# Performance work log

Measured on AMD Instinct MI355X. Metric: run time of the kernel, lower is better.

Reference implementation:

```python
import jax, jax.numpy as jnp
import numpy as np

V, E, H, T = 100000, 128, 256, 7
B, S = 64, 512
START, STOP = 5, 6
H2 = H // 2


def setup_inputs() -> dict:
    key = jax.random.key(0)
    ks = jax.random.split(key, 16)
    rn = lambda k, shape, s=0.1: jax.random.normal(k, shape, jnp.float32) * s
    inp = {}
    inp["sentence"] = jax.random.randint(ks[0], (B, S), 0, V)
    inp["tags"] = jax.random.randint(ks[1], (B, S), 0, 5)
    inp["h0"] = jax.random.normal(ks[2], (2, B, H2), jnp.float32)
    inp["c0"] = jax.random.normal(ks[3], (2, B, H2), jnp.float32)
    inp["embedding"] = rn(ks[4], (V, E), 1.0)
    inp["w_ih_f"] = rn(ks[5], (4 * H2, E)); inp["w_hh_f"] = rn(ks[6], (4 * H2, H2))
    inp["b_ih_f"] = rn(ks[7], (4 * H2,)); inp["b_hh_f"] = rn(ks[8], (4 * H2,))
    inp["w_ih_b"] = rn(ks[9], (4 * H2, E)); inp["w_hh_b"] = rn(ks[10], (4 * H2, H2))
    inp["b_ih_b"] = rn(ks[11], (4 * H2,)); inp["b_hh_b"] = rn(ks[12], (4 * H2,))
    inp["w_out"] = rn(ks[13], (T, H)); inp["b_out"] = rn(ks[14], (T,))
    trans = jax.random.normal(ks[15], (T, T), jnp.float32)
    trans = trans.at[START, :].set(-10000.0).at[:, STOP].set(-10000.0)
    inp["transitions"] = trans
    return inp


def _lstm_dir(x, h0, c0, wih, whh, bih, bhh, reverse):
    # x: [S, B, E]; PyTorch gate order i, f, g, o
    def step(carry, xt):
        h, c = carry
        z = xt @ wih.T + h @ whh.T + bih + bhh  # [B, 4*H2]
        i, f, g, o = jnp.split(z, 4, axis=-1)
        c = jax.nn.sigmoid(f) * c + jax.nn.sigmoid(i) * jnp.tanh(g)
        h = jax.nn.sigmoid(o) * jnp.tanh(c)
        return (h, c), h
    _, hs = jax.lax.scan(step, (h0, c0), x, reverse=reverse)
    return hs  # [S, B, H2]


def reference(sentence, tags, h0, c0, embedding, w_ih_f, w_hh_f, b_ih_f, b_hh_f,
              w_ih_b, w_hh_b, b_ih_b, b_hh_b, w_out, b_out, transitions):
    # Embedding; torch code does .view(S, B, -1) on a [B, S, E] tensor (raw
    # reinterpretation) -- replicate with reshape to match the math exactly.
    embeds = embedding[sentence].reshape(S, B, E)
    hf = _lstm_dir(embeds, h0[0], c0[0], w_ih_f, w_hh_f, b_ih_f, b_hh_f, False)
    hb = _lstm_dir(embeds, h0[1], c0[1], w_ih_b, w_hh_b, b_ih_b, b_hh_b, True)
    feats = jnp.concatenate([hf, hb], axis=-1) @ w_out.T + b_out  # [S, B, T]

    # CRF forward algorithm. Original uses transitions.t(), i.e. step score
    # for prev=i -> next=j is transitions[i, j].
    alpha0 = jnp.full((B, T), -10000.0, jnp.float32).at[:, START].set(0.0)
    def crf_step(alpha, feat):
        # [b, i, j]: alpha[b,i] + transitions[i,j]; LSE over i, add emit[b,j]
        a = jax.nn.logsumexp(alpha[:, :, None] + transitions[None, :, :], axis=1) + feat
        return a, None
    alpha, _ = jax.lax.scan(crf_step, alpha0, feats)
    fwd_score = jax.nn.logsumexp(alpha + transitions[STOP][None, :], axis=1)  # [B]

    # Gold path score: transitions[next, prev] + emit[next], per _score_sentence.
    tags_ext = jnp.concatenate([jnp.full((B, 1), START, tags.dtype), tags], axis=1)
    t_prev, t_next = tags_ext[:, :-1], tags_ext[:, 1:]  # [B, S]
    trans_sc = transitions[t_next, t_prev].sum(axis=1)
    emit_sc = jnp.take_along_axis(jnp.transpose(feats, (1, 0, 2)),
                                  t_next[:, :, None], axis=2)[..., 0].sum(axis=1)
    gold = trans_sc + emit_sc + transitions[STOP, tags_ext[:, -1]]
    return jnp.sum(fwd_score - gold) / B
```

## Files before the change

kernel.cpp:

```cpp
#include <hip/hip_runtime.h>

typedef unsigned int u32;
typedef unsigned short u16;
typedef __attribute__((ext_vector_type(8))) short short8;
typedef __attribute__((ext_vector_type(4))) float f32x4;
typedef __attribute__((ext_vector_type(2))) float f32x2;

#define DEV __device__ __forceinline__
#define LOG2E 1.44269504089f

DEV u16 f2bf(float f) {
    u32 u = __float_as_uint(f);
    return (u16)((u + 0x7FFFu + ((u >> 16) & 1u)) >> 16);
}
DEV float bf2f(u16 h) { return __uint_as_float(((u32)h) << 16); }
DEV float frcp(float x) { return __builtin_amdgcn_rcpf(x); }
DEV float fexp2(float x) {
#if __has_builtin(__builtin_amdgcn_exp2f)
    return __builtin_amdgcn_exp2f(x);
#else
    return exp2f(x);
#endif
}
DEV u32 pack_bf16(float a, float b) {
#if __has_builtin(__builtin_amdgcn_cvt_pk_bf16_f32)
    auto v = __builtin_amdgcn_cvt_pk_bf16_f32(a, b);
    u32 r; __builtin_memcpy(&r, &v, 4); return r;
#else
    return (u32)f2bf(a) | ((u32)f2bf(b) << 16);
#endif
}
DEV float xex(uint2 v, int r) {
    u32 u = (r & 2) ? v.y : v.x;
    return (r & 1) ? __uint_as_float(u & 0xFFFF0000u) : __uint_as_float(u << 16);
}

DEV int gmap2(int g) { return ((g & 3) << 7) + (g & 0x7C) + (g >> 7); }

DEV f32x2 exp2p(f32x2 a) { f32x2 r; r.x = fexp2(a.x); r.y = fexp2(a.y); return r; }
DEV f32x2 rcpp(f32x2 a)  { f32x2 r; r.x = frcp(a.x);  r.y = frcp(a.y);  return r; }
DEV f32x2 minp(f32x2 a, float b) { f32x2 r; r.x = fminf(a.x, b); r.y = fminf(a.y, b); return r; }

DEV f32x2 lstm_pair(f32x2 zi, f32x2 zf, f32x2 zg, f32x2 zo, f32x2* cst) {
    f32x2 ei = exp2p(-zi);
    f32x2 ef = exp2p(-zf);
    f32x2 eo = exp2p(-zo);
    f32x2 eg = exp2p(minp(zg + zg, 115.f));
    f32x2 A = 1.f + ei, F = 1.f + ef, G = eg + 1.f, O = 1.f + eo;
    f32x2 AG = A * G;
    f32x2 cc = (*cst * AG + (eg - 1.f) * F) * rcpp(F * AG);
    *cst = cc;
    f32x2 ec = exp2p(minp(cc * 2.885390082f, 115.f));
    return (ec - 1.f) * rcpp(O * (ec + 1.f));
}

__global__ __launch_bounds__(512) void k_inproj2(
    const int* __restrict__ sent, const float* __restrict__ emb,
    const float* __restrict__ wihf, const float* __restrict__ bihf, const float* __restrict__ bhhf,
    const float* __restrict__ wihb, const float* __restrict__ bihb, const float* __restrict__ bhhb,
    u16* __restrict__ Xf, u16* __restrict__ Xb)
{
    int blk = blockIdx.x;
    int d  = blk >> 8;
    int sc = blk & 255;
    const float* wih = d ? wihb : wihf;
    const float* bih = d ? bihb : bihf;
    const float* bhh = d ? bhhb : bhhf;
    u16* X = d ? Xb : Xf;
    int tid = threadIdx.x;
    int w = tid >> 6, lane = tid & 63;
    int rg = lane >> 4, cn = lane & 15;

    short8 afr[4][4];
    #pragma unroll
    for (int mi = 0; mi < 4; ++mi) {
        int gate = gmap2(16 * (w + 8 * mi) + cn);
        #pragma unroll
        for (int kt = 0; kt < 4; ++kt) {
            const float* p = wih + (size_t)gate * 128 + kt * 32 + rg * 8;
            float4 f0 = *(const float4*)p;
            float4 f1 = *(const float4*)(p + 4);
            union { short8 v; u32 u[4]; } sv;
            sv.u[0] = pack_bf16(f0.x, f0.y);
            sv.u[1] = pack_bf16(f0.z, f0.w);
            sv.u[2] = pack_bf16(f1.x, f1.y);
            sv.u[3] = pack_bf16(f1.z, f1.w);
            afr[mi][kt] = sv.v;
        }
    }
    float bs[4][4];
    #pragma unroll
    for (int mi = 0; mi < 4; ++mi)
        #pragma unroll
        for (int r = 0; r < 4; ++r) {
            int g = gmap2(16 * (w + 8 * mi) + 4 * rg + r);
            bs[mi][r] = bih[g] + bhh[g];
        }

    __shared__ u16 tile[2][64][136];
    {
        int row = tid >> 2, q = tid & 3;
        int sl = row >> 6, bb = row & 63;
        int tok = sent[(sc * 2 + sl) * 64 + bb];
        const float* er = emb + (size_t)tok * 128 + q * 32;
        u16* dst = &tile[sl][bb][q * 32];
        #pragma unroll
        for (int u = 0; u < 4; ++u) {
            float4 a = *(const float4*)(er + u * 8);
            float4 c = *(const float4*)(er + u * 8 + 4);
            uint4 st;
            st.x = pack_bf16(a.x, a.y); st.y = pack_bf16(a.z, a.w);
            st.z = pack_bf16(c.x, c.y); st.w = pack_bf16(c.z, c.w);
            *(uint4*)(dst + u * 8) = st;
        }
    }
    __syncthreads();
    #pragma unroll
    for (int ss = 0; ss < 2; ++ss) {
        int s = sc * 2 + ss;
        #pragma unroll
        for (int nt = 0; nt < 4; ++nt) {
            short8 bfr[4];
            #pragma unroll
            for (int kt = 0; kt < 4; ++kt)
                bfr[kt] = *(const short8*)&tile[ss][nt * 16 + cn][kt * 32 + rg * 8];
            #pragma unroll
            for (int mi = 0; mi < 4; ++mi) {
                f32x4 acc = {0.f, 0.f, 0.f, 0.f};
                #pragma unroll
                for (int kt = 0; kt < 4; ++kt)
                    acc = __builtin_amdgcn_mfma_f32_16x16x32_bf16(afr[mi][kt], bfr[kt], acc, 0, 0, 0);
                size_t base = (((size_t)s * 4 + nt) * 32 + (w + 8 * mi)) * 256
                            + (size_t)rg * 64 + (size_t)cn * 4;
                uint2 st;
                st.x = pack_bf16((acc[0] + bs[mi][0]) * LOG2E, (acc[1] + bs[mi][1]) * LOG2E);
                st.y = pack_bf16((acc[2] + bs[mi][2]) * LOG2E, (acc[3] + bs[mi][3]) * LOG2E);
                *(uint2*)(X + base) = st;
            }
        }
    }
}

__global__ __launch_bounds__(512) void k_lstm(
    const float* __restrict__ h0, const float* __restrict__ c0,
    const float* __restrict__ whhf, const float* __restrict__ whhb,
    const u16* __restrict__ Xf, const u16* __restrict__ Xb,
    u16* __restrict__ hfo, u16* __restrict__ hbo)
{
    int d  = blockIdx.x >> 2, g4 = blockIdx.x & 3;
    const float* whh = d ? whhb : whhf;
    const u16*   X   = d ? Xb   : Xf;
    u16*         ho  = d ? hbo  : hfo;
    int w = threadIdx.x >> 6, lane = threadIdx.x & 63;
    int rg = lane >> 4, cn = lane & 15;

    short8 afr[4][4];
    #pragma unroll
    for (int mi = 0; mi < 4; ++mi) {
        int gate = gmap2(16 * (w + 8 * mi) + cn);
        #pragma unroll
        for (int kt = 0; kt < 4; ++kt) {
            const float* p = whh + (size_t)gate * 128 + kt * 32 + rg * 8;
            float4 f0 = *(const float4*)p;
            float4 f1 = *(const float4*)(p + 4);
            union { short8 v; u32 u[4]; } sv;
            sv.u[0] = pack_bf16(f0.x * LOG2E, f0.y * LOG2E);
            sv.u[1] = pack_bf16(f0.z * LOG2E, f0.w * LOG2E);
            sv.u[2] = pack_bf16(f1.x * LOG2E, f1.y * LOG2E);
            sv.u[3] = pack_bf16(f1.z * LOG2E, f1.w * LOG2E);
            afr[mi][kt] = sv.v;
        }
    }
    int b = g4 * 16 + cn;
    int chb = 16 * w + rg * 4;
    f32x2 cstA, cstB;
    {
        float4 cv = *(const float4*)(c0 + ((size_t)d * 64 + b) * 128 + chb);
        cstA.x = cv.x; cstA.y = cv.y;
        cstB.x = cv.z; cstB.y = cv.w;
    }
    __shared__ u16 hbuf[2][16][136];
    {
        float4 hv = *(const float4*)(h0 + ((size_t)d * 64 + b) * 128 + chb);
        uint2 st0;
        st0.x = pack_bf16(hv.x, hv.y);
        st0.y = pack_bf16(hv.z, hv.w);
        *(uint2*)&hbuf[0][cn][chb] = st0;
    }
    __syncthreads();

    int s0 = d ? 511 : 0;
    const int sdelta = d ? -32768 : 32768;
    const ptrdiff_t hdelta = d ? -8192 : 8192;
    size_t lof = (size_t)rg * 64 + (size_t)cn * 4;

    const u16* pa[4]; const u16* pb[4];
    uint2 xA[4], xB[4];
    #pragma unroll
    for (int mi = 0; mi < 4; ++mi) {
        const u16* base = X + (((size_t)s0 * 4 + g4) * 32 + (w + 8 * mi)) * 256 + lof;
        xA[mi] = *(const uint2*)base;
        xB[mi] = *(const uint2*)(base + sdelta);
        pa[mi] = base + 2 * sdelta;
        pb[mi] = base + 3 * sdelta;
    }
    u16* hop = ho + ((size_t)s0 * 64 + b) * 128 + chb;

#define LSTM_STEP(RB, WB, XC, XP)                                            \
    do {                                                                     \
        short8 bfr[4];                                                       \
        _Pragma("unroll")                                                    \
        for (int kt = 0; kt < 4; ++kt)                                       \
            bfr[kt] = *(const short8*)&hbuf[RB][cn][kt * 32 + rg * 8];       \
        f32x4 z[4];                                                          \
        _Pragma("unroll")                                                    \
        for (int mi = 0; mi < 4; ++mi) {                                     \
            f32x4 acc;                                                       \
            acc[0] = xex(XC[mi], 0); acc[1] = xex(XC[mi], 1);                \
            acc[2] = xex(XC[mi], 2); acc[3] = xex(XC[mi], 3);                \
            _Pragma("unroll")                                                \
            for (int kt = 0; kt < 4; ++kt)                                   \
                acc = __builtin_amdgcn_mfma_f32_16x16x32_bf16(               \
                    afr[mi][kt], bfr[kt], acc, 0, 0, 0);                     \
            z[mi] = acc;                                                     \
            XC[mi] = *(const uint2*)XP[mi];                                  \
            XP[mi] += 2 * sdelta;                                            \
        }                                                                    \
        f32x2 ziA = {z[0][0], z[1][0]}, zfA = {z[0][1], z[1][1]};            \
        f32x2 zgA = {z[0][2], z[1][2]}, zoA = {z[0][3], z[1][3]};            \
        f32x2 hA = lstm_pair(ziA, zfA, zgA, zoA, &cstA);                     \
        u32 pA = pack_bf16(hA.x, hA.y);                                      \
        *(u32*)&hbuf[WB][cn][chb] = pA;                                      \
        *(u32*)hop = pA;                                                     \
        f32x2 ziB = {z[2][0], z[3][0]}, zfB = {z[2][1], z[3][1]};            \
        f32x2 zgB = {z[2][2], z[3][2]}, zoB = {z[2][3], z[3][3]};            \
        f32x2 hB = lstm_pair(ziB, zfB, zgB, zoB, &cstB);                     \
        u32 pB = pack_bf16(hB.x, hB.y);                                      \
        *(u32*)&hbuf[WB][cn][chb + 2] = pB;                                  \
        *(u32*)(hop + 2) = pB;                                               \
        hop += hdelta;                                                       \
        asm volatile("s_waitcnt lgkmcnt(0)\n\ts_barrier" ::: "memory");      \
    } while (0)

    for (int it = 0; it < 256; ++it) {
        LSTM_STEP(0, 1, xA, pa);
        LSTM_STEP(1, 0, xB, pb);
    }
#undef LSTM_STEP
}

__global__ __launch_bounds__(256) void k_feats(
    const u16* __restrict__ hf, const u16* __restrict__ hb,
    const float* __restrict__ wout, const float* __restrict__ bout,
    float* __restrict__ feats)
{
    __shared__ u16 sf[32][136], sb[32][136];
    __shared__ float wo[7][260];
    __shared__ float bo[8];
    int tid = threadIdx.x;
    int pos0 = blockIdx.x * 32;
    {
        int r = tid >> 3, cc = (tid & 7) * 16;
        const uint4* pf = (const uint4*)(hf + (size_t)(pos0 + r) * 128 + cc);
        const uint4* pb = (const uint4*)(hb + (size_t)(pos0 + r) * 128 + cc);
        *(uint4*)&sf[r][cc]     = pf[0];
        *(uint4*)&sf[r][cc + 8] = pf[1];
        *(uint4*)&sb[r][cc]     = pb[0];
        *(uint4*)&sb[r][cc + 8] = pb[1];
    }
    for (int i = tid; i < 1792; i += 256) wo[i >> 8][i & 255] = wout[i];
    if (tid < 7) bo[tid] = bout[tid];
    __syncthreads();
    int pp = tid >> 3, tt = tid & 7;
    if (tt < 7) {
        float acc = bo[tt];
        #pragma unroll 4
        for (int ch = 0; ch < 128; ch += 2) {
            u32 uf = *(const u32*)&sf[pp][ch];
            u32 ub = *(const u32*)&sb[pp][ch];
            float2 w0 = *(const float2*)&wo[tt][ch];
            float2 w1 = *(const float2*)&wo[tt][128 + ch];
            acc += __uint_as_float(uf << 16) * w0.x
                 + __uint_as_float(uf & 0xFFFF0000u) * w0.y
                 + __uint_as_float(ub << 16) * w1.x
                 + __uint_as_float(ub & 0xFFFF0000u) * w1.y;
        }
        feats[(size_t)(pos0 + pp) * 7 + tt] = acc;
    }
}

__global__ __launch_bounds__(64) void k_crf_chunk(
    const float* __restrict__ feats, const float* __restrict__ trans,
    float* __restrict__ chunkM)
{
    int b = blockIdx.x >> 3, c = blockIdx.x & 7;
    int lane = threadIdx.x;
    int i = lane >> 3, j = lane & 7;
    __shared__ float fl[64][8];
    int s0 = c * 64;
    for (int idx = lane; idx < 448; idx += 64) {
        int ss = idx / 7, jj = idx - ss * 7;
        fl[ss][jj] = feats[(size_t)((s0 + ss) * 64 + b) * 7 + jj];
    }
    float tc[7];
    #pragma unroll
    for (int k = 0; k < 7; ++k) tc[k] = (j < 7) ? trans[k * 7 + j] : 0.f;
    bool valid = (i < 7 && j < 7);
    float M0 = valid ? trans[i * 7 + j] : -1e30f;
    __syncthreads();
    float M = M0 + (valid ? fl[0][j] : 0.f);
    for (int ss = 1; ss < 64; ++ss) {
        int rb = i * 8;
        float v0 = __shfl(M, rb + 0, 64) + tc[0];
        float v1 = __shfl(M, rb + 1, 64) + tc[1];
        float v2 = __shfl(M, rb + 2, 64) + tc[2];
        float v3 = __shfl(M, rb + 3, 64) + tc[3];
        float v4 = __shfl(M, rb + 4, 64) + tc[4];
        float v5 = __shfl(M, rb + 5, 64) + tc[5];
        float v6 = __shfl(M, rb + 6, 64) + tc[6];
        float mx = fmaxf(fmaxf(fmaxf(v0, v1), fmaxf(v2, v3)),
                         fmaxf(fmaxf(v4, v5), v6));
        float sm = __expf(v0 - mx) + __expf(v1 - mx) + __expf(v2 - mx)
                 + __expf(v3 - mx) + __expf(v4 - mx) + __expf(v5 - mx)
                 + __expf(v6 - mx);
        M = mx + __logf(sm) + fl[ss][j];
    }
    if (valid)
        chunkM[(size_t)(b * 8 + c) * 49 + i * 7 + j] = M;
}

__global__ __launch_bounds__(512) void k_crf_final(
    const float* __restrict__ chunkM, const float* __restrict__ trans,
    const int* __restrict__ tags, const float* __restrict__ feats,
    float* __restrict__ out)
{
    int tid = threadIdx.x;
    int w = tid >> 6, lane = tid & 63;
    int k = lane >> 3, j = lane & 7;
    int b = w * 8 + k;
    bool jv = (j < 7);
    __shared__ float Tl[49];
    __shared__ float red[512];
    __shared__ float fsh[64];
    if (tid < 49) Tl[tid] = trans[tid];
    __syncthreads();

    float av = (j == 5) ? 0.f : -1e4f;
    #pragma unroll
    for (int c = 0; c < 8; ++c) {
        float a0 = __shfl(av, k * 8 + 0, 64);
        float a1 = __shfl(av, k * 8 + 1, 64);
        float a2 = __shfl(av, k * 8 + 2, 64);
        float a3 = __shfl(av, k * 8 + 3, 64);
        float a4 = __shfl(av, k * 8 + 4, 64);
        float a5 = __shfl(av, k * 8 + 5, 64);
        float a6 = __shfl(av, k * 8 + 6, 64);
        if (jv) {
            const float* Pp = chunkM + ((size_t)b * 8 + c) * 49 + j;
            float v0 = a0 + Pp[0],  v1 = a1 + Pp[7],  v2 = a2 + Pp[14];
            float v3 = a3 + Pp[21], v4 = a4 + Pp[28], v5 = a5 + Pp[35];
            float v6 = a6 + Pp[42];
            float mx = fmaxf(fmaxf(fmaxf(v0, v1), fmaxf(v2, v3)),
                             fmaxf(fmaxf(v4, v5), v6));
            float sm = __expf(v0 - mx) + __expf(v1 - mx) + __expf(v2 - mx)
                     + __expf(v3 - mx) + __expf(v4 - mx) + __expf(v5 - mx)
                     + __expf(v6 - mx);
            av = mx + __logf(sm);
        }
    }
    float u = jv ? (av + Tl[42 + j]) : -1e30f;
    float m = u;
    #pragma unroll
    for (int off = 1; off < 8; off <<= 1) m = fmaxf(m, __shfl_xor(m, off, 64));
    float e = jv ? __expf(u - m) : 0.f;
    #pragma unroll
    for (int off = 1; off < 8; off <<= 1) e += __shfl_xor(e, off, 64);
    float fwd = m + __logf(e);
    if (j == 0) fsh[b] = fwd;

    int tb = tid & 63, q = tid >> 6;
    const int* tgp = tags + (size_t)tb * 512 + q * 64;
    float acc = 0.f;
    int tp = (q == 0) ? 5 : tgp[-1];
    for (int g8 = 0; g8 < 8; ++g8) {
        int4 ta = *(const int4*)(tgp + g8 * 8);
        int4 tb4 = *(const int4*)(tgp + g8 * 8 + 4);
        int t8[8] = {ta.x, ta.y, ta.z, ta.w, tb4.x, tb4.y, tb4.z, tb4.w};
        float f8[8];
        #pragma unroll
        for (int u2 = 0; u2 < 8; ++u2)
            f8[u2] = feats[(size_t)((q * 64 + g8 * 8 + u2) * 64 + tb) * 7 + t8[u2]];
        #pragma unroll
        for (int u2 = 0; u2 < 8; ++u2) {
            acc += Tl[t8[u2] * 7 + tp] + f8[u2];
            tp = t8[u2];
        }
    }
    if (q == 7) acc += Tl[42 + tgp[63]];
    red[tid] = acc;
    __syncthreads();
    if (tid < 64) {
        float g = red[tid];
        #pragma unroll
        for (int qq = 1; qq < 8; ++qq) g += red[tid + 64 * qq];
        red[tid] = fsh[tid] - g;
    }
    __syncthreads();
    if (tid < 64) {
        float v = red[tid];
        #pragma unroll
        for (int off = 1; off < 64; off <<= 1) v += __shfl_xor(v, off, 64);
        if (tid == 0) out[0] = v * (1.0f / 64.0f);
    }
}

extern "C" void kernel_launch(void* const* d_in, const int* in_sizes, int n_in,
                              void* d_out, int out_size, void* d_ws, size_t ws_size,
                              hipStream_t stream) {
    const int*   sent = (const int*)d_in[0];
    const int*   tags = (const int*)d_in[1];
    const float* h0   = (const float*)d_in[2];
    const float* c0   = (const float*)d_in[3];
    const float* emb  = (const float*)d_in[4];
    const float* wihf = (const float*)d_in[5];
    const float* whhf = (const float*)d_in[6];
    const float* bihf = (const float*)d_in[7];
    const float* bhhf = (const float*)d_in[8];
    const float* wihb = (const float*)d_in[9];
    const float* whhb = (const float*)d_in[10];
    const float* bihb = (const float*)d_in[11];
    const float* bhhb = (const float*)d_in[12];
    const float* wout = (const float*)d_in[13];
    const float* bout = (const float*)d_in[14];
    const float* trn  = (const float*)d_in[15];

    char* ws = (char*)d_ws;
    u16*   Xf     = (u16*)(ws);
    u16*   Xb     = (u16*)(ws + 33554432);
    u16*   hfp    = (u16*)(ws + 67108864);
    u16*   hbp    = (u16*)(ws + 75497472);
    float* feats  = (float*)(ws + 83886080);
    float* chunkM = (float*)(ws + 84803584);

    k_inproj2<<<512, 512, 0, stream>>>(sent, emb, wihf, bihf, bhhf,
                                       wihb, bihb, bhhb, Xf, Xb);
    k_lstm<<<8, 512, 0, stream>>>(h0, c0, whhf, whhb, Xf, Xb, hfp, hbp);
    k_feats<<<1024, 256, 0, stream>>>(hfp, hbp, wout, bout, feats);
    k_crf_chunk<<<512, 64, 0, stream>>>(feats, trn, chunkM);
    k_crf_final<<<1, 512, 0, stream>>>(chunkM, trn, tags, feats, (float*)d_out);
}
```

Measured before the change: 566.8 us.

## Fuse input projection and LSTM recurrence with flag-based producer/consumer overlap

Merges the input-projection kernel and the recurrent LSTM kernel into one launch. Blocks 0-7 run the recurrence, and the remaining 512 blocks compute the projected inputs and signal completion of each 16-timestep chunk through atomic flags. The recurrence blocks spin-wait on those flags before consuming each chunk, so the sequential scan can start while projections are still being produced. It adds spin-wait polling, a memset launch and a dependency on the recurrence blocks being co-resident with producers. The flags reuse the feats buffer, which is later overwritten by k_feats.

Result: slower. 613.9 us (+8.3%).

```diff
diff --git a/kernel.cpp b/kernel.cpp
--- a/kernel.cpp
+++ b/kernel.cpp
@@ -54,105 +54,109 @@
     return (ec - 1.f) * rcpp(O * (ec + 1.f));
 }
 
-__global__ __launch_bounds__(512) void k_inproj2(
+__global__ __launch_bounds__(512) void k_fused(
     const int* __restrict__ sent, const float* __restrict__ emb,
     const float* __restrict__ wihf, const float* __restrict__ bihf, const float* __restrict__ bhhf,
     const float* __restrict__ wihb, const float* __restrict__ bihb, const float* __restrict__ bhhb,
-    u16* __restrict__ Xf, u16* __restrict__ Xb)
+    u16* __restrict__ Xf, u16* __restrict__ Xb,
+    const float* __restrict__ h0, const float* __restrict__ c0,
+    const float* __restrict__ whhf, const float* __restrict__ whhb,
+    u16* __restrict__ hfo, u16* __restrict__ hbo,
+    u32* __restrict__ flags)
 {
-    int blk = blockIdx.x;
-    int d  = blk >> 8;
-    int sc = blk & 255;
-    const float* wih = d ? wihb : wihf;
-    const float* bih = d ? bihb : bihf;
-    const float* bhh = d ? bhhb : bhhf;
-    u16* X = d ? Xb : Xf;
+    __shared__ u16 shm[2][64][136];
     int tid = threadIdx.x;
     int w = tid >> 6, lane = tid & 63;
     int rg = lane >> 4, cn = lane & 15;
 
-    short8 afr[4][4];
-    #pragma unroll
-    for (int mi = 0; mi < 4; ++mi) {
-        int gate = gmap2(16 * (w + 8 * mi) + cn);
-        #pragma unroll
-        for (int kt = 0; kt < 4; ++kt) {
-            const float* p = wih + (size_t)gate * 128 + kt * 32 + rg * 8;
-            float4 f0 = *(const float4*)p;
-            float4 f1 = *(const float4*)(p + 4);
-            union { short8 v; u32 u[4]; } sv;
-            sv.u[0] = pack_bf16(f0.x, f0.y);
-            sv.u[1] = pack_bf16(f0.z, f0.w);
-            sv.u[2] = pack_bf16(f1.x, f1.y);
-            sv.u[3] = pack_bf16(f1.z, f1.w);
-            afr[mi][kt] = sv.v;
-        }
-    }
-    float bs[4][4];
-    #pragma unroll
-    for (int mi = 0; mi < 4; ++mi)
-        #pragma unroll
-        for (int r = 0; r < 4; ++r) {
-            int g = gmap2(16 * (w + 8 * mi) + 4 * rg + r);
-            bs[mi][r] = bih[g] + bhh[g];
-        }
-
-    __shared__ u16 tile[2][64][136];
-    {
-        int row = tid >> 2, q = tid & 3;
-        int sl = row >> 6, bb = row & 63;
-        int tok = sent[(sc * 2 + sl) * 64 + bb];
-        const float* er = emb + (size_t)tok * 128 + q * 32;
-        u16* dst = &tile[sl][bb][q * 32];
-        #pragma unroll
-        for (int u = 0; u < 4; ++u) {
-            float4 a = *(const float4*)(er + u * 8);
-            float4 c = *(const float4*)(er + u * 8 + 4);
-            uint4 st;
-            st.x = pack_bf16(a.x, a.y); st.y = pack_bf16(a.z, a.w);
-            st.z = pack_bf16(c.x, c.y); st.w = pack_bf16(c.z, c.w);
-            *(uint4*)(dst + u * 8) = st;
-        }
-    }
-    __syncthreads();
-    #pragma unroll
-    for (int ss = 0; ss < 2; ++ss) {
-        int s = sc * 2 + ss;
-        #pragma unroll
-        for (int nt = 0; nt < 4; ++nt) {
-            short8 bfr[4];
+    if (blockIdx.x >= 8) {
+        int c = blockIdx.x - 8;
+        int d  = c >> 8;
+        int sc = c & 255;
+        const float* wih = d ? wihb : wihf;
+        const float* bih = d ? bihb : bihf;
+        const float* bhh = d ? bhhb : bhhf;
+        u16* X = d ? Xb : Xf;
+
+        short8 afr[4][4];
+        #pragma unroll
+        for (int mi = 0; mi < 4; ++mi) {
+            int gate = gmap2(16 * (w + 8 * mi) + cn);
             #pragma unroll
-            for (int kt = 0; kt < 4; ++kt)
-                bfr[kt] = *(const short8*)&tile[ss][nt * 16 + cn][kt * 32 + rg * 8];
+            for (int kt = 0; kt < 4; ++kt) {
+                const float* p = wih + (size_t)gate * 128 + kt * 32 + rg * 8;
+                float4 f0 = *(const float4*)p;
+                float4 f1 = *(const float4*)(p + 4);
+                union { short8 v; u32 u[4]; } sv;
+                sv.u[0] = pack_bf16(f0.x, f0.y);
+                sv.u[1] = pack_bf16(f0.z, f0.w);
+                sv.u[2] = pack_bf16(f1.x, f1.y);
+                sv.u[3] = pack_bf16(f1.z, f1.w);
+                afr[mi][kt] = sv.v;
+            }
+        }
+        float bs[4][4];
+        #pragma unroll
+        for (int mi = 0; mi < 4; ++mi)
             #pragma unroll
-            for (int mi = 0; mi < 4; ++mi) {
-                f32x4 acc = {0.f, 0.f, 0.f, 0.f};
+            for (int r = 0; r < 4; ++r) {
+                int g = gmap2(16 * (w + 8 * mi) + 4 * rg + r);
+                bs[mi][r] = bih[g] + bhh[g];
+            }
+        {
+            int row = tid >> 2, q = tid & 3;
+            int sl = row >> 6, bb = row & 63;
+            int tok = sent[(sc * 2 + sl) * 64 + bb];
+            const float* er = emb + (size_t)tok * 128 + q * 32;
+            u16* dst = &shm[sl][bb][q * 32];
+            #pragma unroll
+            for (int u = 0; u < 4; ++u) {
+                float4 a = *(const float4*)(er + u * 8);
+                float4 cc = *(const float4*)(er + u * 8 + 4);
+                uint4 st;
+                st.x = pack_bf16(a.x, a.y);  st.y = pack_bf16(a.z, a.w);
+                st.z = pack_bf16(cc.x, cc.y); st.w = pack_bf16(cc.z, cc.w);
+                *(uint4*)(dst + u * 8) = st;
+            }
+        }
+        __syncthreads();
+        #pragma unroll
+        for (int ss = 0; ss < 2; ++ss) {
+            int s = sc * 2 + ss;
+            #pragma unroll
+            for (int nt = 0; nt < 4; ++nt) {
+                short8 bfr[4];
                 #pragma unroll
                 for (int kt = 0; kt < 4; ++kt)
-                    acc = __builtin_amdgcn_mfma_f32_16x16x32_bf16(afr[mi][kt], bfr[kt], acc, 0, 0, 0);
-                size_t base = (((size_t)s * 4 + nt) * 32 + (w + 8 * mi)) * 256
-                            + (size_t)rg * 64 + (size_t)cn * 4;
-                uint2 st;
-                st.x = pack_bf16((acc[0] + bs[mi][0]) * LOG2E, (acc[1] + bs[mi][1]) * LOG2E);
-                st.y = pack_bf16((acc[2] + bs[mi][2]) * LOG2E, (acc[3] + bs[mi][3]) * LOG2E);
-                *(uint2*)(X + base) = st;
+                    bfr[kt] = *(const short8*)&shm[ss][nt * 16 + cn][kt * 32 + rg * 8];
+                #pragma unroll
+                for (int mi = 0; mi < 4; ++mi) {
+                    f32x4 acc = {0.f, 0.f, 0.f, 0.f};
+                    #pragma unroll
+                    for (int kt = 0; kt < 4; ++kt)
+                        acc = __builtin_amdgcn_mfma_f32_16x16x32_bf16(afr[mi][kt], bfr[kt], acc, 0, 0, 0);
+                    size_t base = (((size_t)s * 4 + nt) * 32 + (w + 8 * mi)) * 256
+                                + (size_t)rg * 64 + (size_t)cn * 4;
+                    uint2 st;
+                    st.x = pack_bf16((acc[0] + bs[mi][0]) * LOG2E, (acc[1] + bs[mi][1]) * LOG2E);
+                    st.y = pack_bf16((acc[2] + bs[mi][2]) * LOG2E, (acc[3] + bs[mi][3]) * LOG2E);
+                    *(uint2*)(X + base) = st;
+                }
             }
         }
-    }
-}
-
-__global__ __launch_bounds__(512) void k_lstm(
-    const float* __restrict__ h0, const float* __restrict__ c0,
-    const float* __restrict__ whhf, const float* __restrict__ whhb,
-    const u16* __restrict__ Xf, const u16* __restrict__ Xb,
-    u16* __restrict__ hfo, u16* __restrict__ hbo)
-{
+        __syncthreads();
+        if (tid == 0)
+            __hip_atomic_fetch_add(&flags[(d << 5) | (sc >> 3)], 1u,
+                                   __ATOMIC_RELEASE, __HIP_MEMORY_SCOPE_AGENT);
+        return;
+    }
+
+    __builtin_amdgcn_s_setprio(1);
     int d  = blockIdx.x >> 2, g4 = blockIdx.x & 3;
     const float* whh = d ? whhb : whhf;
     const u16*   X   = d ? Xb   : Xf;
     u16*         ho  = d ? hbo  : hfo;
-    int w = threadIdx.x >> 6, lane = threadIdx.x & 63;
-    int rg = lane >> 4, cn = lane & 15;
+    u16 (*hbuf)[16][136] = (u16(*)[16][136])&shm[0][0][0];
 
     short8 afr[4][4];
     #pragma unroll
@@ -179,7 +183,6 @@
         cstA.x = cv.x; cstA.y = cv.y;
         cstB.x = cv.z; cstB.y = cv.w;
     }
-    __shared__ u16 hbuf[2][16][136];
     {
         float4 hv = *(const float4*)(h0 + ((size_t)d * 64 + b) * 128 + chb);
         uint2 st0;
@@ -193,6 +196,13 @@
     const int sdelta = d ? -32768 : 32768;
     const ptrdiff_t hdelta = d ? -8192 : 8192;
     size_t lof = (size_t)rg * 64 + (size_t)cn * 4;
+
+#define WAITC(p)                                                             \
+    while (__hip_atomic_load(&flags[(d << 5) | (p)], __ATOMIC_ACQUIRE,       \
+                             __HIP_MEMORY_SCOPE_AGENT) < 8u)                 \
+        __builtin_amdgcn_s_sleep(8)
+
+    WAITC(d ? 31 : 0);
 
     const u16* pa[4]; const u16* pb[4];
     uint2 xA[4], xB[4];
@@ -243,10 +253,15 @@
     } while (0)
 
     for (int it = 0; it < 256; ++it) {
+        if ((it & 7) == 6) {
+            int m = (it + 2) >> 3; if (m > 31) m = 31;
+            WAITC(d ? (31 - m) : m);
+        }
         LSTM_STEP(0, 1, xA, pa);
         LSTM_STEP(1, 0, xB, pb);
     }
 #undef LSTM_STEP
+#undef WAITC
 }
 
 __global__ __launch_bounds__(256) void k_feats(
@@ -441,10 +456,12 @@
     u16*   hbp    = (u16*)(ws + 75497472);
     float* feats  = (float*)(ws + 83886080);
     float* chunkM = (float*)(ws + 84803584);
-
-    k_inproj2<<<512, 512, 0, stream>>>(sent, emb, wihf, bihf, bhhf,
-                                       wihb, bihb, bhhb, Xf, Xb);
-    k_lstm<<<8, 512, 0, stream>>>(h0, c0, whhf, whhb, Xf, Xb, hfp, hbp);
+    u32*   flags  = (u32*)feats;
+
+    hipMemsetAsync(flags, 0, 256, stream);
+    k_fused<<<520, 512, 0, stream>>>(sent, emb, wihf, bihf, bhhf,
+                                     wihb, bihb, bhhb, Xf, Xb,
+                                     h0, c0, whhf, whhb, hfp, hbp, flags);
     k_feats<<<1024, 256, 0, stream>>>(hfp, hbp, wout, bout, feats);
     k_crf_chunk<<<512, 64, 0, stream>>>(feats, trn, chunkM);
     k_crf_final<<<1, 512, 0, stream>>>(chunkM, trn, tags, feats, (float*)d_out);
```
